# Kernel tuning notes

Measured on AMD Instinct MI355X. Metric: run time of the kernel, lower is better.

## Reference

```python
import jax, jax.numpy as jnp
import numpy as np

B, L, C, H = 2, 2048, 2048, 16
COND = 2048
HID = 4 * C
LN_EPS = 1e-6


def _ln(x):
    m = jnp.mean(x, axis=-1, keepdims=True)
    v = jnp.mean((x - m) ** 2, axis=-1, keepdims=True)
    return (x - m) / jnp.sqrt(v + LN_EPS)


def _gelu_tanh(u):
    c = np.sqrt(2.0 / np.pi).astype(np.float32)
    return 0.5 * u * (1.0 + jnp.tanh(c * (u + 0.044715 * u ** 3)))


def setup_inputs() -> dict:
    key = jax.random.key(0)
    ks = jax.random.split(key, 8)
    s = 0.02
    return {
        "x": jax.random.normal(ks[0], (B, L, C), jnp.float32),
        "cond_BD": jax.random.normal(ks[1], (B, COND), jnp.float32),
        "attn_bias": jnp.zeros((1, 1, L, L), jnp.float32),
        "Wqkv": (jax.random.normal(ks[2], (3 * C, C), jnp.float32) * s),
        "q_bias": jnp.zeros((C,), jnp.float32),
        "v_bias": jnp.zeros((C,), jnp.float32),
        "scale_mul_log": jnp.full((1, H, 1, 1), np.log(4.0), jnp.float32),
        "Wproj": (jax.random.normal(ks[3], (C, C), jnp.float32) * s),
        "bproj": jnp.zeros((C,), jnp.float32),
        "Wada": (jax.random.normal(ks[4], (6 * C, COND), jnp.float32) * s),
        "bada": jnp.zeros((6 * C,), jnp.float32),
        "Wfc1": (jax.random.normal(ks[5], (HID, C), jnp.float32) * s),
        "bfc1": jnp.zeros((HID,), jnp.float32),
        "Wfc2": (jax.random.normal(ks[6], (C, HID), jnp.float32) * s),
        "bfc2": jnp.zeros((C,), jnp.float32),
    }


def reference(x, cond_BD, attn_bias, Wqkv, q_bias, v_bias, scale_mul_log,
              Wproj, bproj, Wada, bada, Wfc1, bfc1, Wfc2, bfc2):
    Bs, Lx, Cx = x.shape
    D = Cx // H
    # AdaLN modulation: SiLU -> Linear(cond_dim, 6C) -> view(B,1,6,C).unbind(2)
    ada = (jax.nn.silu(cond_BD) @ Wada.T + bada).reshape(Bs, 1, 6, Cx)
    gamma1, gamma2, scale1, scale2, shift1, shift2 = [ada[:, :, i, :] for i in range(6)]

    def attn(xin):
        qkv_bias = jnp.concatenate([q_bias, jnp.zeros_like(q_bias), v_bias])
        qkv = (xin @ Wqkv.T + qkv_bias).reshape(Bs, Lx, 3, H, D)
        qkv = jnp.transpose(qkv, (2, 0, 3, 1, 4))  # [3, B, H, L, D]
        q, k, v = qkv[0], qkv[1], qkv[2]
        # cos-attn: L2-normalize q,k; q scaled by exp(clamped log-scale); softmax scale = 1
        sm = jnp.exp(jnp.minimum(scale_mul_log, jnp.log(jnp.float32(100.0))))
        qn = q / jnp.maximum(jnp.linalg.norm(q, axis=-1, keepdims=True), 1e-12) * sm
        kn = k / jnp.maximum(jnp.linalg.norm(k, axis=-1, keepdims=True), 1e-12)
        scores = jnp.einsum('bhqd,bhkd->bhqk', qn, kn) + attn_bias
        p = jax.nn.softmax(scores, axis=-1)
        o = jnp.einsum('bhqk,bhkd->bhqd', p, v)
        o = jnp.transpose(o, (0, 2, 1, 3)).reshape(Bs, Lx, Cx)
        return o @ Wproj.T + bproj

    x = x + attn(_ln(x) * (scale1 + 1.0) + shift1) * gamma1
    h = _gelu_tanh((_ln(x) * (scale2 + 1.0) + shift2) @ Wfc1.T + bfc1)
    x = x + (h @ Wfc2.T + bfc2) * gamma2
    return x
```

## Files before the change

### kernel.cpp

```cpp
#include <hip/hip_runtime.h>

typedef unsigned short u16;
typedef float f32x4 __attribute__((ext_vector_type(4)));
typedef short short8 __attribute__((ext_vector_type(8)));

#define C_ 2048
#define L_ 2048
#define H_ 16
#define D_ 128
#define SIXC 12288

__device__ __forceinline__ u16 f2bf(float f) {
  union { float f; unsigned u; } v; v.f = f;
  unsigned r = v.u + 0x7FFFu + ((v.u >> 16) & 1u);
  return (u16)(r >> 16);
}
__device__ __forceinline__ float bf2f(u16 b) {
  union { unsigned u; float f; } v; v.u = ((unsigned)b) << 16; return v.f;
}

#define GLOAD_LDS16(g, l)                                            \
  __builtin_amdgcn_global_load_lds(                                  \
      (__attribute__((address_space(1))) void*)(g),                  \
      (__attribute__((address_space(3))) void*)(l), 16, 0, 0)

template <int N> __device__ __forceinline__ void wait_vmcnt() {
  if constexpr (N == 8)      asm volatile("s_waitcnt vmcnt(8)" ::: "memory");
  else if constexpr (N == 6) asm volatile("s_waitcnt vmcnt(6)" ::: "memory");
  else                       asm volatile("s_waitcnt vmcnt(0)" ::: "memory");
}

__global__ __launch_bounds__(256) void conv_bf16(
    const float* __restrict__ src, u16* __restrict__ dst, int n) {
  int i = (blockIdx.x * 256 + threadIdx.x) * 4;
  if (i >= n) return;
  float4 v = *(const float4*)&src[i];
  ushort4 o;
  o.x = f2bf(v.x); o.y = f2bf(v.y); o.z = f2bf(v.z); o.w = f2bf(v.w);
  *(ushort4*)&dst[i] = o;
}

__global__ __launch_bounds__(256) void prep_kernel(
    const float* __restrict__ cond, const float* __restrict__ qb,
    const float* __restrict__ vb, const float* __restrict__ sml,
    float* __restrict__ silu_cond, float* __restrict__ qkvbias,
    float* __restrict__ sm) {
  int i = blockIdx.x * 256 + threadIdx.x;
  if (i < 4096) { float c = cond[i]; silu_cond[i] = c / (1.f + __expf(-c)); }
  if (i < 6144) {
    float bv = (i < 2048) ? qb[i] : ((i < 4096) ? 0.f : vb[i - 4096]);
    qkvbias[i] = bv;
  }
  if (i < 16) sm[i] = __expf(fminf(sml[i], 4.6051701859880914f));
}

__global__ __launch_bounds__(256) void ada_gemm(
    const float* __restrict__ sc, const float* __restrict__ Wada,
    const float* __restrict__ bada, float* __restrict__ ada) {
  int gw = (blockIdx.x * 256 + threadIdx.x) >> 6;
  int lane = threadIdx.x & 63;
  int b = gw / SIXC, row = gw % SIXC;
  const float* s0 = sc + b * 2048;
  const float* w0 = Wada + (size_t)row * 2048;
  float s = 0.f;
  for (int k = lane * 4; k < 2048; k += 256) {
    float4 a = *(const float4*)&s0[k];
    float4 w = *(const float4*)&w0[k];
    s = fmaf(a.x, w.x, s); s = fmaf(a.y, w.y, s);
    s = fmaf(a.z, w.z, s); s = fmaf(a.w, w.w, s);
  }
  #pragma unroll
  for (int off = 32; off; off >>= 1) s += __shfl_xor(s, off);
  if (lane == 0) ada[(size_t)b * SIXC + row] = s + bada[row];
}

__global__ __launch_bounds__(256) void ln_mod(
    const float* __restrict__ x, const float* __restrict__ ada,
    u16* __restrict__ out, int soff, int shoff) {
  int r = blockIdx.x;
  int b = r >> 11;
  int tid = threadIdx.x;
  const float* xr = x + (size_t)r * 2048;
  int c0 = tid * 8;
  float4 u0 = *(const float4*)&xr[c0];
  float4 u1 = *(const float4*)&xr[c0 + 4];
  float v[8] = {u0.x,u0.y,u0.z,u0.w,u1.x,u1.y,u1.z,u1.w};
  float s = 0.f, s2 = 0.f;
  #pragma unroll
  for (int j = 0; j < 8; ++j) { s += v[j]; s2 = fmaf(v[j], v[j], s2); }
  int wv = tid >> 6, lane = tid & 63;
  #pragma unroll
  for (int off = 32; off; off >>= 1) { s += __shfl_xor(s, off); s2 += __shfl_xor(s2, off); }
  __shared__ float red[8];
  if (!lane) { red[wv] = s; red[4 + wv] = s2; }
  __syncthreads();
  s = red[0] + red[1] + red[2] + red[3];
  s2 = red[4] + red[5] + red[6] + red[7];
  float mean = s * (1.f / 2048.f);
  float var = s2 * (1.f / 2048.f) - mean * mean;
  float rstd = rsqrtf(var + 1e-6f);
  const float* sc = ada + (size_t)b * SIXC + soff;
  const float* sh = ada + (size_t)b * SIXC + shoff;
  u16* orow = out + (size_t)r * 2048;
  #pragma unroll
  for (int j = 0; j < 8; ++j) {
    int c = c0 + j;
    float y = (v[j] - mean) * rstd * (1.f + sc[c]) + sh[c];
    orow[c] = f2bf(y);
  }
}

__global__ __launch_bounds__(256) void qk_norm_bf(
    u16* __restrict__ qb, u16* __restrict__ kb, const float* __restrict__ sm) {
  int gw = (blockIdx.x * 256 + threadIdx.x) >> 6;
  int lane = threadIdx.x & 63;
  int which = gw >> 16;
  int rid = gw & 0xFFFF;
  int h = (rid >> 11) & 15;
  u16* base = (which ? kb : qb) + (size_t)rid * 128 + lane * 2;
  unsigned uu = *(const unsigned*)base;
  float v0 = bf2f((u16)(uu & 0xFFFFu));
  float v1 = bf2f((u16)(uu >> 16));
  float ss = v0 * v0 + v1 * v1;
  #pragma unroll
  for (int off = 32; off; off >>= 1) ss += __shfl_xor(ss, off);
  float rn = 1.f / fmaxf(sqrtf(ss), 1e-12f);
  if (which == 0) rn *= sm[h];
  unsigned o = (unsigned)f2bf(v0 * rn) | ((unsigned)f2bf(v1 * rn) << 16);
  *(unsigned*)base = o;
}

#define PSP 68
__global__ __launch_bounds__(256) void attn_mfma(
    const u16* __restrict__ qb, const u16* __restrict__ kb,
    const u16* __restrict__ vbt, const float* __restrict__ bias,
    u16* __restrict__ o) {
  __shared__ u16 Ks[2][64 * 128];
  __shared__ u16 Vt[2][128 * 64];
  __shared__ u16 Ps[4][16 * PSP];
  int tid = threadIdx.x;
  int w = tid >> 6, lane = tid & 63;
  int flat = blockIdx.y * gridDim.x + blockIdx.x;
  int rl = (flat & 7) * 128 + (flat >> 3);
  int bh = rl >> 5, b = bh >> 4, h = bh & 15;
  int q0 = (rl & 31) * 64;
  int lr = lane & 15, lg = lane >> 4;
  short8 aq[4];
  {
    const u16* qrow = qb + ((size_t)bh * L_ + q0 + w * 16 + lr) * 128 + lg * 8;
    #pragma unroll
    for (int ks = 0; ks < 4; ++ks) aq[ks] = *(const short8*)(qrow + ks * 32);
  }
  f32x4 oacc[8] = {};
  float m = -1e30f, l = 0.f;
  const float* brow = bias + (size_t)(q0 + w * 16 + lr) * L_;
  const u16* kbase = kb + (size_t)bh * L_ * 128;
  const u16* vbase = vbt + (size_t)bh * 128 * L_;
  const int kq0 = tid;
  const int vq0 = tid;

  float4 brg[4], bnr[4];
  #pragma unroll
  for (int i = 0; i < 4; ++i) {
    int q = i * 256 + kq0;
    int r = q >> 4, c = q & 15;
    GLOAD_LDS16(kbase + (size_t)r * 128 + ((c ^ (r & 7)) * 8), &Ks[0][q * 8]);
  }
  #pragma unroll
  for (int i = 0; i < 4; ++i) {
    int q = i * 256 + vq0;
    int r = q >> 3, c = q & 7;
    GLOAD_LDS16(vbase + (size_t)r * L_ + ((c ^ (r & 7)) * 8), &Vt[0][q * 8]);
  }
  #pragma unroll
  for (int kg = 0; kg < 4; ++kg)
    brg[kg] = *(const float4*)&brow[kg * 16 + lg * 4];
  __syncthreads();

  for (int kt = 0; kt < 32; ++kt) {
    const int cur = kt & 1;
    if (kt < 31) {
      const int nxt = cur ^ 1;
      const u16* kb2 = kbase + (size_t)(kt + 1) * 64 * 128;
      #pragma unroll
      for (int i = 0; i < 4; ++i) {
        int q = i * 256 + kq0;
        int r = q >> 4, c = q & 15;
        GLOAD_LDS16(kb2 + (size_t)r * 128 + ((c ^ (r & 7)) * 8), &Ks[nxt][q * 8]);
      }
      #pragma unroll
      for (int i = 0; i < 4; ++i) {
        int q = i * 256 + vq0;
        int r = q >> 3, c = q & 7;
        GLOAD_LDS16(vbase + (size_t)r * L_ + (kt + 1) * 64 + ((c ^ (r & 7)) * 8),
                    &Vt[nxt][q * 8]);
      }
      #pragma unroll
      for (int kg = 0; kg < 4; ++kg)
        bnr[kg] = *(const float4*)&brow[(kt + 1) * 64 + kg * 16 + lg * 4];
    }
    f32x4 s[4] = {};
    __builtin_amdgcn_s_setprio(1);
    #pragma unroll
    for (int ks = 0; ks < 4; ++ks) {
      #pragma unroll
      for (int kg = 0; kg < 4; ++kg) {
        int row = kg * 16 + lr;
        short8 bk = *(const short8*)&Ks[cur][row * 128 + (((ks * 4 + lg) ^ (lr & 7)) * 8)];
        s[kg] = __builtin_amdgcn_mfma_f32_16x16x32_bf16(bk, aq[ks], s[kg], 0, 0, 0);
      }
    }
    __builtin_amdgcn_s_setprio(0);
    float p[4][4];
    #pragma unroll
    for (int kg = 0; kg < 4; ++kg) {
      p[kg][0] = s[kg][0] + brg[kg].x;
      p[kg][1] = s[kg][1] + brg[kg].y;
      p[kg][2] = s[kg][2] + brg[kg].z;
      p[kg][3] = s[kg][3] + brg[kg].w;
    }
    float tm = fmaxf(
        fmaxf(fmaxf(fmaxf(p[0][0], p[0][1]), fmaxf(p[0][2], p[0][3])),
              fmaxf(fmaxf(p[1][0], p[1][1]), fmaxf(p[1][2], p[1][3]))),
        fmaxf(fmaxf(fmaxf(p[2][0], p[2][1]), fmaxf(p[2][2], p[2][3])),
              fmaxf(fmaxf(p[3][0], p[3][1]), fmaxf(p[3][2], p[3][3]))));
    tm = fmaxf(tm, __shfl_xor(tm, 16));
    tm = fmaxf(tm, __shfl_xor(tm, 32));
    if (__any(tm > m + 8.f)) {
      float nm = fmaxf(m, tm);
      float a = __expf(m - nm);
      m = nm;
      l *= a;
      float al[4];
      #pragma unroll
      for (int j = 0; j < 4; ++j) al[j] = __shfl(a, lg * 4 + j);
      #pragma unroll
      for (int dg = 0; dg < 8; ++dg) {
        f32x4 t = oacc[dg];
        t[0] *= al[0]; t[1] *= al[1]; t[2] *= al[2]; t[3] *= al[3];
        oacc[dg] = t;
      }
    }
    float ps = 0.f;
    #pragma unroll
    for (int kg = 0; kg < 4; ++kg) {
      #pragma unroll
      for (int j = 0; j < 4; ++j) { p[kg][j] = __expf(p[kg][j] - m); ps += p[kg][j]; }
    }
    ps += __shfl_xor(ps, 16);
    ps += __shfl_xor(ps, 32);
    l += ps;
    #pragma unroll
    for (int kg = 0; kg < 4; ++kg) {
      unsigned lo = (unsigned)f2bf(p[kg][0]) | ((unsigned)f2bf(p[kg][1]) << 16);
      unsigned hi = (unsigned)f2bf(p[kg][2]) | ((unsigned)f2bf(p[kg][3]) << 16);
      uint2 w2; w2.x = lo; w2.y = hi;
      *(uint2*)&Ps[w][lr * PSP + kg * 16 + lg * 4] = w2;
    }
    __threadfence_block();
    short8 pa0 = *(const short8*)&Ps[w][lr * PSP + lg * 8];
    short8 pa1 = *(const short8*)&Ps[w][lr * PSP + 32 + lg * 8];
    __builtin_amdgcn_s_setprio(1);
    #pragma unroll
    for (int dg = 0; dg < 8; ++dg) {
      int row = dg * 16 + lr;
      short8 bv0 = *(const short8*)&Vt[cur][row * 64 + ((lg ^ (lr & 7)) * 8)];
      oacc[dg] = __builtin_amdgcn_mfma_f32_16x16x32_bf16(pa0, bv0, oacc[dg], 0, 0, 0);
      short8 bv1 = *(const short8*)&Vt[cur][row * 64 + (((4 + lg) ^ (lr & 7)) * 8)];
      oacc[dg] = __builtin_amdgcn_mfma_f32_16x16x32_bf16(pa1, bv1, oacc[dg], 0, 0, 0);
    }
    __builtin_amdgcn_s_setprio(0);
    __syncthreads();
    #pragma unroll
    for (int i = 0; i < 4; ++i) brg[i] = bnr[i];
  }
  float inv[4];
  #pragma unroll
  for (int j = 0; j < 4; ++j) inv[j] = 1.f / __shfl(l, lg * 4 + j);
  #pragma unroll
  for (int j = 0; j < 4; ++j) {
    u16* dst = &o[((size_t)(b * L_) + q0 + w * 16 + lg * 4 + j) * 2048 + h * 128 + lr];
    #pragma unroll
    for (int dg = 0; dg < 8; ++dg) dst[dg * 16] = f2bf(oacc[dg][j] * inv[j]);
  }
}

template <int EPI>
__global__ __launch_bounds__(256) void gemm128(
    const u16* __restrict__ A, const u16* __restrict__ W,
    const float* __restrict__ bias, const float* __restrict__ res,
    const float* __restrict__ ada, int goff,
    float* __restrict__ outf, u16* __restrict__ outb,
    u16* __restrict__ p0, u16* __restrict__ p1, u16* __restrict__ p2,
    int M, int N, int K) {
  __shared__ u16 As[2][128 * 64];
  __shared__ u16 Bs[2][128 * 64];
  const int tid = threadIdx.x;
  const int nwg = gridDim.x * gridDim.y;
  const int flat = blockIdx.y * gridDim.x + blockIdx.x;
  const int swz = (flat & 7) * (nwg >> 3) + (flat >> 3);
  const int m0 = (swz / gridDim.x) * 128, n0 = (swz % gridDim.x) * 128;
  const int wv = tid >> 6, lane = tid & 63;
  const int wr = wv >> 1, wc = wv & 1;
  const int lr = lane & 15, lg = lane >> 4;
  const int sr = lane >> 3;
  const int scol = ((lane & 7) ^ sr) * 8;
  const int cswz = (lr & 7) * 8;
  f32x4 acc[4][4] = {};
  const u16* Ab = A + (size_t)m0 * K;
  const u16* Bb = W + (size_t)n0 * K;
  const int nt = K >> 6;
  auto stage = [&](int bi, int k0) {
    #pragma unroll
    for (int p = 0; p < 4; ++p) {
      int chunk = wv * 4 + p;
      int row = chunk * 8 + sr;
      GLOAD_LDS16(Ab + (size_t)row * K + k0 + scol, &As[bi][chunk * 512]);
      GLOAD_LDS16(Bb + (size_t)row * K + k0 + scol, &Bs[bi][chunk * 512]);
    }
  };
  stage(0, 0);
  stage(1, 64);
  for (int t = 0; t < nt; ++t) {
    const int cur = t & 1;
    if (t + 1 < nt) wait_vmcnt<8>(); else wait_vmcnt<0>();
    __builtin_amdgcn_s_barrier();
    __builtin_amdgcn_sched_barrier(0);
    #pragma unroll
    for (int kk = 0; kk < 2; ++kk) {
      short8 af[4], bfr[4];
      const int col = (kk * 32 + lg * 8) ^ cswz;
      #pragma unroll
      for (int i = 0; i < 4; ++i) {
        af[i]  = *(const short8*)&As[cur][(wr * 64 + i * 16 + lr) * 64 + col];
        bfr[i] = *(const short8*)&Bs[cur][(wc * 64 + i * 16 + lr) * 64 + col];
      }
      #pragma unroll
      for (int mi = 0; mi < 4; ++mi)
        #pragma unroll
        for (int ni = 0; ni < 4; ++ni)
          acc[mi][ni] = __builtin_amdgcn_mfma_f32_16x16x32_bf16(af[mi], bfr[ni], acc[mi][ni], 0, 0, 0);
    }
    __builtin_amdgcn_sched_barrier(0);
    asm volatile("s_waitcnt lgkmcnt(0)" ::: "memory");
    __builtin_amdgcn_s_barrier();
    __builtin_amdgcn_sched_barrier(0);
    if (t + 2 < nt) stage(cur, (t + 2) << 6);
  }
  #pragma unroll
  for (int mi = 0; mi < 4; ++mi) {
    #pragma unroll
    for (int ni = 0; ni < 4; ++ni) {
      int gcol = n0 + wc * 64 + ni * 16 + lr;
      float bv = bias[gcol];
      #pragma unroll
      for (int j = 0; j < 4; ++j) {
        int grow = m0 + wr * 64 + mi * 16 + lg * 4 + j;
        float v = acc[mi][ni][j] + bv;
        if (EPI == 0) {
          int which = gcol >> 11;
          int h = (gcol >> 7) & 15;
          int d = gcol & 127;
          int b = grow >> 11, ll = grow & 2047;
          int bh = b * 16 + h;
          if (which == 0)      p0[((size_t)bh * L_ + ll) * 128 + d] = f2bf(v);
          else if (which == 1) p1[((size_t)bh * L_ + ll) * 128 + d] = f2bf(v);
          else                 p2[((size_t)bh * 128 + d) * L_ + ll] = f2bf(v);
        } else if (EPI == 1) {
          float u = 0.7978845608028654f * (v + 0.044715f * v * v * v);
          float e = __expf(2.f * u);
          float th = 1.f - 2.f / (e + 1.f);
          outb[(size_t)grow * N + gcol] = f2bf(0.5f * v * (1.f + th));
        } else {
          int b = grow >> 11;
          float g = ada[(size_t)b * SIXC + goff + gcol];
          size_t oi = (size_t)grow * N + gcol;
          outf[oi] = res[oi] + v * g;
        }
      }
    }
  }
}

extern "C" void kernel_launch(void* const* d_in, const int* in_sizes, int n_in,
                              void* d_out, int out_size, void* d_ws, size_t ws_size,
                              hipStream_t stream) {
  const float* x        = (const float*)d_in[0];
  const float* cond     = (const float*)d_in[1];
  const float* attnbias = (const float*)d_in[2];
  const float* Wqkv     = (const float*)d_in[3];
  const float* q_bias   = (const float*)d_in[4];
  const float* v_bias   = (const float*)d_in[5];
  const float* sml      = (const float*)d_in[6];
  const float* Wproj    = (const float*)d_in[7];
  const float* bproj    = (const float*)d_in[8];
  const float* Wada     = (const float*)d_in[9];
  const float* bada     = (const float*)d_in[10];
  const float* Wfc1     = (const float*)d_in[11];
  const float* bfc1     = (const float*)d_in[12];
  const float* Wfc2     = (const float*)d_in[13];
  const float* bfc2     = (const float*)d_in[14];
  float* out = (float*)d_out;
  char* ws = (char*)d_ws;
  const size_t MB = 1ull << 20;

  float* silu_cond = (float*)(ws + 0);
  float* qkvbias   = (float*)(ws + (16 << 10));
  float* smbuf     = (float*)(ws + (40 << 10));
  float* adab      = (float*)(ws + (48 << 10));
  u16*   xob       = (u16*)(ws + 1 * MB);
  u16*   qbb       = (u16*)(ws + 17 * MB);
  u16*   kbb       = (u16*)(ws + 33 * MB);
  float* x1        = (float*)(ws + 17 * MB);
  u16*   vbt       = (u16*)(ws + 49 * MB);
  u16*   hbuf      = (u16*)(ws + 49 * MB);
  u16*   wqkv_bf   = (u16*)(ws + 65 * MB);
  u16*   wproj_bf  = (u16*)(ws + 89 * MB);
  u16*   wfc1_bf   = (u16*)(ws + 113 * MB);
  u16*   wfc2_bf   = (u16*)(ws + 145 * MB);

  conv_bf16<<<12288, 256, 0, stream>>>(Wqkv, wqkv_bf, 6144 * 2048);
  conv_bf16<<<4096, 256, 0, stream>>>(Wproj, wproj_bf, 2048 * 2048);
  conv_bf16<<<16384, 256, 0, stream>>>(Wfc1, wfc1_bf, 8192 * 2048);
  conv_bf16<<<16384, 256, 0, stream>>>(Wfc2, wfc2_bf, 2048 * 8192);
  prep_kernel<<<24, 256, 0, stream>>>(cond, q_bias, v_bias, sml, silu_cond, qkvbias, smbuf);
  ada_gemm<<<6144, 256, 0, stream>>>(silu_cond, Wada, bada, adab);
  ln_mod<<<4096, 256, 0, stream>>>(x, adab, xob, 2 * C_, 4 * C_);
  gemm128<0><<<dim3(48, 32), 256, 0, stream>>>(xob, wqkv_bf, qkvbias, nullptr, nullptr, 0,
                                               nullptr, nullptr, qbb, kbb, vbt, 4096, 6144, 2048);
  qk_norm_bf<<<32768, 256, 0, stream>>>(qbb, kbb, smbuf);
  attn_mfma<<<dim3(32, 32), 256, 0, stream>>>(qbb, kbb, vbt, attnbias, xob);
  gemm128<2><<<dim3(16, 32), 256, 0, stream>>>(xob, wproj_bf, bproj, x, adab, 0,
                                               x1, nullptr, nullptr, nullptr, nullptr, 4096, 2048, 2048);
  ln_mod<<<4096, 256, 0, stream>>>(x1, adab, xob, 3 * C_, 5 * C_);
  gemm128<1><<<dim3(64, 32), 256, 0, stream>>>(xob, wfc1_bf, bfc1, nullptr, nullptr, 0,
                                               nullptr, hbuf, nullptr, nullptr, nullptr, 4096, 8192, 2048);
  gemm128<2><<<dim3(16, 32), 256, 0, stream>>>(hbuf, wfc2_bf, bfc2, x1, adab, C_,
                                               out, nullptr, nullptr, nullptr, nullptr, 4096, 2048, 8192);
}
```

Before: 812.4 us.

## Use 256x256 GEMM tiles for QKV/FC1 and split-K FC2 with combine

Adds a 512-thread gemm256 kernel with 256x256 tiles and a finer-grained schedule that interleaves LDS reads, async global-to-LDS loads and MFMA quarters. The QKV and FC1 GEMMs now use it, raising per-block data reuse. FC2 is split into two K halves so its smaller output still fills the grid, writing bf16 partials that a new fc2_combine kernel sums with bias, gamma and residual. The gemm128 block-index swizzle is also removed. Risks include extra partial-result traffic, bf16 rounding of the partials, and higher register and LDS pressure in the larger tile.

```diff
diff --git a/kernel.cpp b/kernel.cpp
--- a/kernel.cpp
+++ b/kernel.cpp
@@ -285,21 +285,176 @@
   }
 }
 
+#define RD_A(cur, mh)                                                         \
+  _Pragma("unroll") for (int kk = 0; kk < 2; ++kk) {                          \
+    const int col_ = (kk * 32 + lg * 8) ^ cswz;                               \
+    _Pragma("unroll") for (int i = 0; i < 4; ++i)                             \
+      af[i][kk] = *(const short8*)                                            \
+          &As[cur][(wr * 128 + (mh) * 64 + i * 16 + lr) * 64 + col_];         \
+  }
+#define RD_B(cur, nh, BB)                                                     \
+  _Pragma("unroll") for (int kk = 0; kk < 2; ++kk) {                          \
+    const int col_ = (kk * 32 + lg * 8) ^ cswz;                               \
+    _Pragma("unroll") for (int j = 0; j < 2; ++j)                             \
+      BB[j][kk] = *(const short8*)                                            \
+          &Bs[cur][(wc * 64 + (nh) * 32 + j * 16 + lr) * 64 + col_];          \
+  }
+#define MMQ(mh, nh, BB)                                                       \
+  __builtin_amdgcn_s_setprio(1);                                              \
+  _Pragma("unroll") for (int kk = 0; kk < 2; ++kk)                            \
+  _Pragma("unroll") for (int i = 0; i < 4; ++i)                               \
+  _Pragma("unroll") for (int j = 0; j < 2; ++j)                               \
+    acc[(mh) * 4 + i][(nh) * 2 + j] = __builtin_amdgcn_mfma_f32_16x16x32_bf16(\
+        af[i][kk], BB[j][kk], acc[(mh) * 4 + i][(nh) * 2 + j], 0, 0, 0);      \
+  __builtin_amdgcn_s_setprio(0);
+#define LGKM0 asm volatile("s_waitcnt lgkmcnt(0)" ::: "memory")
+
+template <int EPI>
+__global__ __launch_bounds__(512, 2) void gemm256(
+    const u16* __restrict__ A, const u16* __restrict__ W,
+    const float* __restrict__ bias,
+    u16* __restrict__ outb,
+    u16* __restrict__ p0, u16* __restrict__ p1, u16* __restrict__ p2,
+    int M, int N, int K, int lda) {
+  __shared__ __attribute__((aligned(16))) u16 As[2][256 * 64];
+  __shared__ __attribute__((aligned(16))) u16 Bs[2][256 * 64];
+  const int tid = threadIdx.x;
+  int my = blockIdx.y, half = 0;
+  if constexpr (EPI == 3) { half = my >> 4; my &= 15; }
+  const int m0 = my * 256, n0 = blockIdx.x * 256;
+  const int wv = tid >> 6, lane = tid & 63;
+  const int wr = wv >> 2, wc = wv & 3;
+  const int lr = lane & 15, lg = lane >> 4;
+  const int sr = lane >> 3;
+  const int scol = ((lane & 7) ^ sr) * 8;
+  const int cswz = (lr & 7) * 8;
+  f32x4 acc[8][4] = {};
+  const u16* Ab = A + (size_t)m0 * lda + (size_t)half * K;
+  const u16* Bb = W + (size_t)n0 * lda + (size_t)half * K;
+  const int nt = K >> 6;
+
+  auto stA2 = [&](int bi, int k0, int sel) {
+    #pragma unroll
+    for (int q = 0; q < 2; ++q) {
+      int c = wv * 2 + q;
+      int chunk = sel == 0 ? (c < 8 ? c : c + 8)
+                           : (c < 8 ? c + 8 : c + 16);
+      int row = chunk * 8 + sr;
+      GLOAD_LDS16(Ab + (size_t)row * lda + k0 + scol, &As[bi][chunk * 512]);
+    }
+  };
+  auto stA4 = [&](int bi, int k0) {
+    #pragma unroll
+    for (int q = 0; q < 4; ++q) {
+      int chunk = wv * 4 + q, row = chunk * 8 + sr;
+      GLOAD_LDS16(Ab + (size_t)row * lda + k0 + scol, &As[bi][chunk * 512]);
+    }
+  };
+  auto stB4 = [&](int bi, int k0) {
+    #pragma unroll
+    for (int q = 0; q < 4; ++q) {
+      int chunk = wv * 4 + q, row = chunk * 8 + sr;
+      GLOAD_LDS16(Bb + (size_t)row * lda + k0 + scol, &Bs[bi][chunk * 512]);
+    }
+  };
+
+  short8 af[4][2], bfl[2][2], bfh[2][2];
+  stA4(0, 0); stB4(0, 0);
+  stA4(1, 64); stB4(1, 64);
+  wait_vmcnt<8>();
+  __builtin_amdgcn_s_barrier();
+
+  for (int t = 0; t < nt; ++t) {
+    const int cur = t & 1;
+    const int k2 = (t + 2) << 6;
+    const bool st = t + 2 < nt;
+    RD_A(cur, 0); RD_B(cur, 0, bfl);
+    __builtin_amdgcn_s_barrier();
+    LGKM0;
+    MMQ(0, 0, bfl);
+    __builtin_amdgcn_s_barrier();
+    RD_B(cur, 1, bfh);
+    __builtin_amdgcn_s_barrier();
+    LGKM0;
+    if (st) stA2(cur, k2, 0);
+    MMQ(0, 1, bfh);
+    __builtin_amdgcn_s_barrier();
+    RD_A(cur, 1);
+    __builtin_amdgcn_s_barrier();
+    LGKM0;
+    if (st) stB4(cur, k2);
+    MMQ(1, 0, bfl);
+    __builtin_amdgcn_s_barrier();
+    __builtin_amdgcn_sched_barrier(0x10F);
+    if (st) { stA2(cur, k2, 1); wait_vmcnt<8>(); }
+    else if (t + 1 < nt) { wait_vmcnt<0>(); }
+    MMQ(1, 1, bfh);
+    __builtin_amdgcn_s_barrier();
+  }
+
+  #pragma unroll
+  for (int mi = 0; mi < 8; ++mi) {
+    #pragma unroll
+    for (int ni = 0; ni < 4; ++ni) {
+      int gcol = n0 + wc * 64 + ni * 16 + lr;
+      float bv = (EPI == 3) ? 0.f : bias[gcol];
+      #pragma unroll
+      for (int j = 0; j < 4; ++j) {
+        int grow = m0 + wr * 128 + mi * 16 + lg * 4 + j;
+        float v = acc[mi][ni][j] + bv;
+        if constexpr (EPI == 0) {
+          int which = gcol >> 11;
+          int h = (gcol >> 7) & 15;
+          int d = gcol & 127;
+          int b = grow >> 11, ll = grow & 2047;
+          int bh = b * 16 + h;
+          if (which == 0)      p0[((size_t)bh * L_ + ll) * 128 + d] = f2bf(v);
+          else if (which == 1) p1[((size_t)bh * L_ + ll) * 128 + d] = f2bf(v);
+          else                 p2[((size_t)bh * 128 + d) * L_ + ll] = f2bf(v);
+        } else if constexpr (EPI == 1) {
+          float u = 0.7978845608028654f * (v + 0.044715f * v * v * v);
+          float e = __expf(2.f * u);
+          float th = 1.f - 2.f / (e + 1.f);
+          outb[(size_t)grow * N + gcol] = f2bf(0.5f * v * (1.f + th));
+        } else {
+          u16* pd = half ? p1 : p0;
+          pd[(size_t)grow * N + gcol] = f2bf(v);
+        }
+      }
+    }
+  }
+}
+
+__global__ __launch_bounds__(256) void fc2_combine(
+    const u16* __restrict__ pa, const u16* __restrict__ pb,
+    const float* __restrict__ bias, const float* __restrict__ res,
+    const float* __restrict__ ada, float* __restrict__ out) {
+  int i = (blockIdx.x * 256 + threadIdx.x) * 4;
+  int col = i & 2047;
+  int b = i >> 22;
+  ushort4 a4 = *(const ushort4*)&pa[i];
+  ushort4 b4 = *(const ushort4*)&pb[i];
+  float4 r = *(const float4*)&res[i];
+  const float* ad = ada + (size_t)b * SIXC + C_;
+  float4 o;
+  o.x = r.x + (bf2f(a4.x) + bf2f(b4.x) + bias[col])     * ad[col];
+  o.y = r.y + (bf2f(a4.y) + bf2f(b4.y) + bias[col + 1]) * ad[col + 1];
+  o.z = r.z + (bf2f(a4.z) + bf2f(b4.z) + bias[col + 2]) * ad[col + 2];
+  o.w = r.w + (bf2f(a4.w) + bf2f(b4.w) + bias[col + 3]) * ad[col + 3];
+  *(float4*)&out[i] = o;
+}
+
 template <int EPI>
 __global__ __launch_bounds__(256) void gemm128(
     const u16* __restrict__ A, const u16* __restrict__ W,
     const float* __restrict__ bias, const float* __restrict__ res,
     const float* __restrict__ ada, int goff,
     float* __restrict__ outf, u16* __restrict__ outb,
-    u16* __restrict__ p0, u16* __restrict__ p1, u16* __restrict__ p2,
     int M, int N, int K) {
   __shared__ u16 As[2][128 * 64];
   __shared__ u16 Bs[2][128 * 64];
   const int tid = threadIdx.x;
-  const int nwg = gridDim.x * gridDim.y;
-  const int flat = blockIdx.y * gridDim.x + blockIdx.x;
-  const int swz = (flat & 7) * (nwg >> 3) + (flat >> 3);
-  const int m0 = (swz / gridDim.x) * 128, n0 = (swz % gridDim.x) * 128;
+  const int m0 = blockIdx.y * 128, n0 = blockIdx.x * 128;
   const int wv = tid >> 6, lane = tid & 63;
   const int wr = wv >> 1, wc = wv & 1;
   const int lr = lane & 15, lg = lane >> 4;
@@ -357,16 +512,7 @@
       for (int j = 0; j < 4; ++j) {
         int grow = m0 + wr * 64 + mi * 16 + lg * 4 + j;
         float v = acc[mi][ni][j] + bv;
-        if (EPI == 0) {
-          int which = gcol >> 11;
-          int h = (gcol >> 7) & 15;
-          int d = gcol & 127;
-          int b = grow >> 11, ll = grow & 2047;
-          int bh = b * 16 + h;
-          if (which == 0)      p0[((size_t)bh * L_ + ll) * 128 + d] = f2bf(v);
-          else if (which == 1) p1[((size_t)bh * L_ + ll) * 128 + d] = f2bf(v);
-          else                 p2[((size_t)bh * 128 + d) * L_ + ll] = f2bf(v);
-        } else if (EPI == 1) {
+        if (EPI == 1) {
           float u = 0.7978845608028654f * (v + 0.044715f * v * v * v);
           float e = __expf(2.f * u);
           float th = 1.f - 2.f / (e + 1.f);
@@ -396,8 +542,8 @@
   const float* bproj    = (const float*)d_in[8];
   const float* Wada     = (const float*)d_in[9];
   const float* bada     = (const float*)d_in[10];
+  const float* bfc1     = (const float*)d_in[12];
   const float* Wfc1     = (const float*)d_in[11];
-  const float* bfc1     = (const float*)d_in[12];
   const float* Wfc2     = (const float*)d_in[13];
   const float* bfc2     = (const float*)d_in[14];
   float* out = (float*)d_out;
@@ -418,6 +564,8 @@
   u16*   wproj_bf  = (u16*)(ws + 89 * MB);
   u16*   wfc1_bf   = (u16*)(ws + 113 * MB);
   u16*   wfc2_bf   = (u16*)(ws + 145 * MB);
+  u16*   pa        = (u16*)(ws + 1 * MB);
+  u16*   pb        = (u16*)(ws + 113 * MB);
 
   conv_bf16<<<12288, 256, 0, stream>>>(Wqkv, wqkv_bf, 6144 * 2048);
   conv_bf16<<<4096, 256, 0, stream>>>(Wproj, wproj_bf, 2048 * 2048);
@@ -426,15 +574,16 @@
   prep_kernel<<<24, 256, 0, stream>>>(cond, q_bias, v_bias, sml, silu_cond, qkvbias, smbuf);
   ada_gemm<<<6144, 256, 0, stream>>>(silu_cond, Wada, bada, adab);
   ln_mod<<<4096, 256, 0, stream>>>(x, adab, xob, 2 * C_, 4 * C_);
-  gemm128<0><<<dim3(48, 32), 256, 0, stream>>>(xob, wqkv_bf, qkvbias, nullptr, nullptr, 0,
-                                               nullptr, nullptr, qbb, kbb, vbt, 4096, 6144, 2048);
+  gemm256<0><<<dim3(24, 16), 512, 0, stream>>>(xob, wqkv_bf, qkvbias,
+      nullptr, qbb, kbb, vbt, 4096, 6144, 2048, 2048);
   qk_norm_bf<<<32768, 256, 0, stream>>>(qbb, kbb, smbuf);
   attn_mfma<<<dim3(32, 32), 256, 0, stream>>>(qbb, kbb, vbt, attnbias, xob);
   gemm128<2><<<dim3(16, 32), 256, 0, stream>>>(xob, wproj_bf, bproj, x, adab, 0,
-                                               x1, nullptr, nullptr, nullptr, nullptr, 4096, 2048, 2048);
+      x1, nullptr, 4096, 2048, 2048);
   ln_mod<<<4096, 256, 0, stream>>>(x1, adab, xob, 3 * C_, 5 * C_);
-  gemm128<1><<<dim3(64, 32), 256, 0, stream>>>(xob, wfc1_bf, bfc1, nullptr, nullptr, 0,
-                                               nullptr, hbuf, nullptr, nullptr, nullptr, 4096, 8192, 2048);
-  gemm128<2><<<dim3(16, 32), 256, 0, stream>>>(hbuf, wfc2_bf, bfc2, x1, adab, C_,
-                                               out, nullptr, nullptr, nullptr, nullptr, 4096, 2048, 8192);
-}
+  gemm256<1><<<dim3(32, 16), 512, 0, stream>>>(xob, wfc1_bf, bfc1,
+      hbuf, nullptr, nullptr, nullptr, 4096, 8192, 2048, 2048);
+  gemm256<3><<<dim3(8, 32), 512, 0, stream>>>(hbuf, wfc2_bf, bfc2,
+      nullptr, pa, pb, nullptr, 4096, 2048, 4096, 8192);
+  fc2_combine<<<8192, 256, 0, stream>>>(pa, pb, bfc2, x1, adab, out);
+}
```

Measured after the change: 778.8 us. 4.1% less time.
